# Kernel optimization log

Measured on AMD Instinct MI355X. Metric: run time of the kernel, lower is better.

The kernel has to match this reference:

```python
import jax, jax.numpy as jnp
import numpy as np

TOPK = 6
E = 512
IN = 384
M = 8192
LN_EPS = 1e-5


def _lin(x, w, b):
    # torch nn.Linear: y = x @ W^T + b, W is [out, in]
    return x @ w.T + b


def setup_inputs() -> dict:
    key = jax.random.key(0)
    ks = jax.random.split(key, 16)
    s = lambda k, sh: (jax.random.normal(k, sh, dtype=jnp.float32) * 0.02)
    return {
        "x": jax.random.normal(ks[0], (1, M, IN), dtype=jnp.float32),
        "fc1_w": s(ks[1], (E, IN)), "fc1_b": jnp.zeros((E,), jnp.float32),
        "wh_w": s(ks[2], (E, E)),   "wh_b": jnp.zeros((E,), jnp.float32),
        "wt_w": s(ks[3], (E, E)),   "wt_b": jnp.zeros((E,), jnp.float32),
        "l1_w": s(ks[4], (E, E)),   "l1_b": jnp.zeros((E,), jnp.float32),
        "l2_w": s(ks[5], (E, E)),   "l2_b": jnp.zeros((E,), jnp.float32),
        "a1_w": s(ks[6], (E // 2, E)), "a1_b": jnp.zeros((E // 2,), jnp.float32),
        "a2_w": s(ks[7], (1, E // 2)), "a2_b": jnp.zeros((1,), jnp.float32),
        "ln_g": jnp.ones((E,), jnp.float32), "ln_b": jnp.zeros((E,), jnp.float32),
    }


def reference(x, fc1_w, fc1_b, wh_w, wh_b, wt_w, wt_b,
              l1_w, l1_b, l2_w, l2_b, a1_w, a1_b, a2_w, a2_b, ln_g, ln_b):
    lrelu = jax.nn.leaky_relu  # slope 0.01 == torch default
    h = lrelu(_lin(x, fc1_w, fc1_b))                      # [B,M,E]
    h = (h + h.mean(axis=1, keepdims=True)) * 0.5
    e_h = _lin(h, wh_w, wh_b)                             # [B,M,E]
    e_t = _lin(h, wt_w, wt_b)                             # [B,M,E]
    scale = E ** (-0.5)
    attn_logit = (e_h * scale) @ jnp.swapaxes(e_t, -2, -1)  # [B,M,M]
    topk_weight, topk_index = jax.lax.top_k(attn_logit, TOPK)  # [B,M,K]
    # gather top-k neighbor tail embeddings: [B,M,K,E]
    Nb_h = jax.vmap(lambda et, idx: et[idx])(e_t, topk_index)
    topk_prob = jax.nn.softmax(topk_weight, axis=2)       # [B,M,K]
    eh_r = topk_prob[..., None] * Nb_h + (1.0 - topk_prob)[..., None] * e_h[:, :, None, :]
    gate = jnp.tanh(e_h[:, :, None, :] + eh_r)            # [B,M,K,E]
    # faithful to torch einsum('ijkl,ijkm->ijk'): sums l and m independently
    ka_weight = Nb_h.sum(axis=-1) * gate.sum(axis=-1)     # [B,M,K]
    ka_prob = jax.nn.softmax(ka_weight, axis=2)           # [B,M,K]
    e_Nh = jnp.einsum('bmk,bmke->bme', ka_prob, Nb_h)     # [B,M,E]
    sum_emb = lrelu(_lin(e_h + e_Nh, l1_w, l1_b))
    bi_emb = lrelu(_lin(e_h * e_Nh, l2_w, l2_b))
    emb = sum_emb + bi_emb                                # [B,M,E] (dropout = eval identity)
    hn = emb[0]                                           # squeeze(0) -> [M,E]
    # GeoGlobalAttention readout: gate_nn = Linear->LeakyReLU->Linear, softmax over nodes
    g = _lin(lrelu(_lin(hn, a1_w, a1_b)), a2_w, a2_b)     # [M,1]
    att = jax.nn.softmax(g, axis=0)
    pooled = (att * hn).sum(axis=0, keepdims=True)        # [1,E]
    mu = pooled.mean(axis=-1, keepdims=True)
    var = jnp.mean((pooled - mu) ** 2, axis=-1, keepdims=True)
    out = (pooled - mu) / jnp.sqrt(var + LN_EPS) * ln_g + ln_b
    return out
```

## Files before the change

kernel.cpp:

```cpp
#include <hip/hip_runtime.h>
#include <math.h>
#include <stdint.h>

#define M_NODES 8192
#define E_DIM   512
#define NTOPK   6
#define ATTN_SCALE 0.04419417382415922f
#define NEG_BIG (-1e38f)
#define CAND_CAP 192

typedef __attribute__((ext_vector_type(8))) short short8;
typedef __attribute__((ext_vector_type(4))) float f32x4;

__device__ __forceinline__ float lrelu(float v) { return v > 0.f ? v : 0.01f * v; }

__device__ __forceinline__ unsigned short f2bf(float f) {
  uint32_t u = __float_as_uint(f);
  uint32_t r = (u + 0x7FFFu + ((u >> 16) & 1u)) >> 16;
  return (unsigned short)r;
}
__device__ __forceinline__ float bf2f(unsigned short s) {
  return __uint_as_float(((uint32_t)s) << 16);
}

__device__ __forceinline__ void async_cp16(const void* gptr, void* lds) {
  auto g1 = reinterpret_cast<const __attribute__((address_space(1))) unsigned int*>(
      reinterpret_cast<uintptr_t>(gptr));
  auto l3 = reinterpret_cast<__attribute__((address_space(3))) unsigned int*>(
      reinterpret_cast<uintptr_t>(lds));
  __builtin_amdgcn_global_load_lds(g1, l3, 16, 0, 0);
}



__global__ __launch_bounds__(256) void wcast_kernel(
    const float* __restrict__ x, const float* __restrict__ fc1w,
    const float* __restrict__ whw, const float* __restrict__ wtw,
    const float* __restrict__ l1w, const float* __restrict__ l2w,
    const float* __restrict__ a1w,
    unsigned short* __restrict__ xT, unsigned short* __restrict__ fc1T,
    unsigned short* __restrict__ whT, unsigned short* __restrict__ wtT,
    unsigned short* __restrict__ l1T, unsigned short* __restrict__ l2T,
    unsigned short* __restrict__ a1T)
{
  const int gid = blockIdx.x * 256 + threadIdx.x;
  const float* src; unsigned short* dst; int K8, local;
  if (gid < 417792) {
    K8 = 48;
    if (gid < 393216) { src = x; dst = xT; local = gid; }
    else { src = fc1w; dst = fc1T; local = gid - 393216; }
  } else {
    K8 = 64;
    if (gid < 450560)      { src = whw; dst = whT; local = gid - 417792; }
    else if (gid < 483328) { src = wtw; dst = wtT; local = gid - 450560; }
    else if (gid < 516096) { src = l1w; dst = l1T; local = gid - 483328; }
    else if (gid < 548864) { src = l2w; dst = l2T; local = gid - 516096; }
    else                   { src = a1w; dst = a1T; local = gid - 548864; }
  }
  const int m = local / K8;
  const int k8 = local - m * K8;
  const float* p = src + (size_t)m * (K8 * 8) + k8 * 8;
  float4 v0 = ((const float4*)p)[0];
  float4 v1 = ((const float4*)p)[1];
  const int Kt = K8 >> 2;
  const size_t ti = ((size_t)(m >> 4) * Kt + (k8 >> 2)) * 512 + ((m & 15) + 16 * (k8 & 3)) * 8;
  uint4 pk;
  pk.x = (uint32_t)f2bf(v0.x) | ((uint32_t)f2bf(v0.y) << 16);
  pk.y = (uint32_t)f2bf(v0.z) | ((uint32_t)f2bf(v0.w) << 16);
  pk.z = (uint32_t)f2bf(v1.x) | ((uint32_t)f2bf(v1.y) << 16);
  pk.w = (uint32_t)f2bf(v1.z) | ((uint32_t)f2bf(v1.w) << 16);
  *(uint4*)(dst + ti) = pk;
}

__global__ __launch_bounds__(256, 4) void gemm1_kernel(
    const unsigned short* __restrict__ xT, const unsigned short* __restrict__ fc1T,
    const float* __restrict__ b1, unsigned short* __restrict__ hT,
    float* __restrict__ colsum)
{
  __shared__ unsigned short As[8 * 512];
  __shared__ unsigned short Bs[8 * 512];
  const int tid = threadIdx.x, lane = tid & 63, w = tid >> 6;
  const int wr = w >> 1, wc = w & 1;
  const int m0 = blockIdx.y * 128;
  const int n0 = blockIdx.x * 128;

  f32x4 acc[4][4];
#pragma unroll
  for (int i = 0; i < 4; i++)
#pragma unroll
    for (int j = 0; j < 4; j++) acc[i][j] = (f32x4){0.f, 0.f, 0.f, 0.f};

  for (int kt = 0; kt < 12; kt++) {
    const int s0 = w, s1 = w + 4;
    async_cp16(xT + ((size_t)((m0 >> 4) + s0) * 12 + kt) * 512 + lane * 8, &As[s0 * 512]);
    async_cp16(xT + ((size_t)((m0 >> 4) + s1) * 12 + kt) * 512 + lane * 8, &As[s1 * 512]);
    async_cp16(fc1T + ((size_t)((n0 >> 4) + s0) * 12 + kt) * 512 + lane * 8, &Bs[s0 * 512]);
    async_cp16(fc1T + ((size_t)((n0 >> 4) + s1) * 12 + kt) * 512 + lane * 8, &Bs[s1 * 512]);
    __syncthreads();
    short8 a[4], b[4];
#pragma unroll
    for (int i = 0; i < 4; i++) a[i] = *(const short8*)&As[(wr * 4 + i) * 512 + lane * 8];
#pragma unroll
    for (int j = 0; j < 4; j++) b[j] = *(const short8*)&Bs[(wc * 4 + j) * 512 + lane * 8];
#pragma unroll
    for (int i = 0; i < 4; i++)
#pragma unroll
      for (int j = 0; j < 4; j++)
        acc[i][j] = __builtin_amdgcn_mfma_f32_16x16x32_bf16(a[i], b[j], acc[i][j], 0, 0, 0);
    __syncthreads();
  }

  const int q = lane >> 4, lcol = lane & 15;
  float colp[4] = {};
#pragma unroll
  for (int i = 0; i < 4; i++)
#pragma unroll
    for (int j = 0; j < 4; j++) {
      const int c = n0 + wc * 64 + j * 16 + lcol;
      const float bias = b1[c];
#pragma unroll
      for (int d = 0; d < 4; d++) {
        const int r = m0 + wr * 64 + i * 16 + q * 4 + d;
        const float v = 0.5f * lrelu(acc[i][j][d] + bias);
        hT[((size_t)(r >> 4) * 16 + (c >> 5)) * 512 +
           ((r & 15) + 16 * ((c >> 3) & 3)) * 8 + (c & 7)] = f2bf(v);
        colp[j] += v;
      }
    }
#pragma unroll
  for (int j = 0; j < 4; j++) {
    colp[j] += __shfl_xor(colp[j], 16);
    colp[j] += __shfl_xor(colp[j], 32);
  }
  if (lane < 16) {
#pragma unroll
    for (int j = 0; j < 4; j++)
      atomicAdd(&colsum[n0 + wc * 64 + j * 16 + lcol], colp[j]);
  }
}

__global__ __launch_bounds__(256) void meanproj_kernel(
    const float* __restrict__ colsum, const float* __restrict__ whw,
    const float* __restrict__ wtw, const float* __restrict__ whb,
    const float* __restrict__ wtb, float* __restrict__ biasHT)
{
  const int lane = threadIdx.x & 63;
  const int c1024 = blockIdx.x * 4 + (threadIdx.x >> 6);
  const bool isH = c1024 < 512;
  const int c = isH ? c1024 : c1024 - 512;
  const float* W = (isH ? whw : wtw) + (size_t)c * 512 + lane * 8;
  const float* cs = colsum + lane * 8;
  float s = 0.f;
#pragma unroll
  for (int e = 0; e < 8; e++) s = fmaf(cs[e], W[e], s);
#pragma unroll
  for (int off = 32; off; off >>= 1) s += __shfl_xor(s, off);
  if (lane == 0)
    biasHT[c1024] = (isH ? whb : wtb)[c] + s * (1.f / (float)M_NODES);
}

__global__ __launch_bounds__(256, 4) void dual_gemm(
    const unsigned short* __restrict__ hT, const unsigned short* __restrict__ wstackT,
    const float* __restrict__ biasHT,
    unsigned short* __restrict__ ehT, unsigned short* __restrict__ etT,
    unsigned short* __restrict__ ehRow, unsigned short* __restrict__ etRow)
{
  __shared__ unsigned short As[8 * 512];
  __shared__ unsigned short Bs[8 * 512];
  const int tid = threadIdx.x, lane = tid & 63, w = tid >> 6;
  const int wr = w >> 1, wc = w & 1;
  const int m0 = blockIdx.y * 128;
  const int n0 = blockIdx.x * 128;

  f32x4 acc[4][4];
#pragma unroll
  for (int i = 0; i < 4; i++)
#pragma unroll
    for (int j = 0; j < 4; j++) acc[i][j] = (f32x4){0.f, 0.f, 0.f, 0.f};

  for (int kt = 0; kt < 16; kt++) {
    const int s0 = w, s1 = w + 4;
    async_cp16(hT + ((size_t)((m0 >> 4) + s0) * 16 + kt) * 512 + lane * 8, &As[s0 * 512]);
    async_cp16(hT + ((size_t)((m0 >> 4) + s1) * 16 + kt) * 512 + lane * 8, &As[s1 * 512]);
    async_cp16(wstackT + ((size_t)((n0 >> 4) + s0) * 16 + kt) * 512 + lane * 8, &Bs[s0 * 512]);
    async_cp16(wstackT + ((size_t)((n0 >> 4) + s1) * 16 + kt) * 512 + lane * 8, &Bs[s1 * 512]);
    __syncthreads();
    short8 a[4], b[4];
#pragma unroll
    for (int i = 0; i < 4; i++) a[i] = *(const short8*)&As[(wr * 4 + i) * 512 + lane * 8];
#pragma unroll
    for (int j = 0; j < 4; j++) b[j] = *(const short8*)&Bs[(wc * 4 + j) * 512 + lane * 8];
#pragma unroll
    for (int i = 0; i < 4; i++)
#pragma unroll
      for (int j = 0; j < 4; j++)
        acc[i][j] = __builtin_amdgcn_mfma_f32_16x16x32_bf16(a[i], b[j], acc[i][j], 0, 0, 0);
    __syncthreads();
  }

  const int q = lane >> 4, lcol = lane & 15;
  const bool isH = (n0 < 512);
  const int cb = isH ? n0 : (n0 - 512);
  unsigned short* T = isH ? ehT : etT;
  unsigned short* R = isH ? ehRow : etRow;

#pragma unroll
  for (int i = 0; i < 4; i++)
#pragma unroll
    for (int j = 0; j < 4; j++) {
      const int cl = wc * 64 + j * 16 + lcol;
      const float bias = biasHT[n0 + cl];
      const int c = cb + cl;
#pragma unroll
      for (int d = 0; d < 4; d++) {
        const int r = m0 + wr * 64 + i * 16 + q * 4 + d;
        const unsigned short us = f2bf(acc[i][j][d] + bias);
        T[((size_t)(r >> 4) * 16 + (c >> 5)) * 512 +
          ((r & 15) + 16 * ((c >> 3) & 3)) * 8 + (c & 7)] = us;
        R[(size_t)r * E_DIM + c] = us;
      }
    }
}

template <int MODE>
__global__ __launch_bounds__(256) void mfma_gemm(
    const unsigned short* __restrict__ At1, const unsigned short* __restrict__ At2,
    const unsigned short* __restrict__ Wt1, const unsigned short* __restrict__ Wt2,
    const float* __restrict__ b1, const float* __restrict__ b2,
    float* __restrict__ Cf, unsigned short* __restrict__ T1,
    unsigned short* __restrict__ Cbf, int N, int K)
{
  constexpr bool DUALW = (MODE == 2);
  __shared__ unsigned short As[2][8 * 512];
  __shared__ unsigned short Bs[2][4 * 512];
  const int Kt = K >> 5;
  const int tid = threadIdx.x, lane = tid & 63, w = tid >> 6;
  const int m0 = blockIdx.y * 128, n0 = blockIdx.x * 64;

  f32x4 acc0[2][4], acc1[2][4];
#pragma unroll
  for (int p = 0; p < 2; p++)
#pragma unroll
    for (int j = 0; j < 4; j++) {
      acc0[p][j] = (f32x4){0.f, 0.f, 0.f, 0.f};
      acc1[p][j] = (f32x4){0.f, 0.f, 0.f, 0.f};
    }

  for (int kt = 0; kt < Kt; kt++) {
    const unsigned short* a1p = At1 + ((size_t)((m0 >> 4) + 2 * w) * Kt + kt) * 512 + lane * 8;
    async_cp16(a1p, &As[0][(2 * w) * 512]);
    async_cp16(a1p + (size_t)Kt * 512, &As[0][(2 * w + 1) * 512]);
    if (MODE == 2) {
      const unsigned short* a2p = At2 + ((size_t)((m0 >> 4) + 2 * w) * Kt + kt) * 512 + lane * 8;
      async_cp16(a2p, &As[1][(2 * w) * 512]);
      async_cp16(a2p + (size_t)Kt * 512, &As[1][(2 * w + 1) * 512]);
    }
    const unsigned short* bp1 = Wt1 + ((size_t)((n0 >> 4) + w) * Kt + kt) * 512 + lane * 8;
    async_cp16(bp1, &Bs[0][w * 512]);
    if (DUALW) {
      const unsigned short* bp2 = Wt2 + ((size_t)((n0 >> 4) + w) * Kt + kt) * 512 + lane * 8;
      async_cp16(bp2, &Bs[1][w * 512]);
    }
    __syncthreads();
    short8 a[2], a2[2], bb[4], bb2[4];
#pragma unroll
    for (int p = 0; p < 2; p++) a[p] = *(const short8*)&As[0][(2 * w + p) * 512 + lane * 8];
    if (MODE == 2) {
#pragma unroll
      for (int p = 0; p < 2; p++) a2[p] = *(const short8*)&As[1][(2 * w + p) * 512 + lane * 8];
    }
#pragma unroll
    for (int j = 0; j < 4; j++) bb[j] = *(const short8*)&Bs[0][j * 512 + lane * 8];
    if (DUALW) {
#pragma unroll
      for (int j = 0; j < 4; j++) bb2[j] = *(const short8*)&Bs[1][j * 512 + lane * 8];
    }
#pragma unroll
    for (int p = 0; p < 2; p++)
#pragma unroll
      for (int j = 0; j < 4; j++) {
        acc0[p][j] = __builtin_amdgcn_mfma_f32_16x16x32_bf16(a[p], bb[j], acc0[p][j], 0, 0, 0);
        if (MODE == 2)
          acc1[p][j] = __builtin_amdgcn_mfma_f32_16x16x32_bf16(a2[p], bb2[j], acc1[p][j], 0, 0, 0);
      }
    __syncthreads();
  }

  const int lrow = (lane >> 4) * 4, lcol = lane & 15;

  if (MODE == 3) {
    float part[2][4] = {};
#pragma unroll
    for (int p = 0; p < 2; p++)
#pragma unroll
      for (int j = 0; j < 4; j++) {
        const int c = n0 + j * 16 + lcol;
        const float bias1 = b1[c];
        const float w2 = b2[c];
#pragma unroll
        for (int d = 0; d < 4; d++)
          part[p][d] = fmaf(lrelu(acc0[p][j][d] + bias1), w2, part[p][d]);
      }
#pragma unroll
    for (int p = 0; p < 2; p++)
#pragma unroll
      for (int d = 0; d < 4; d++) {
#pragma unroll
        for (int off = 1; off < 16; off <<= 1)
          part[p][d] += __shfl_xor(part[p][d], off);
      }
    if (lcol == 0) {
#pragma unroll
      for (int p = 0; p < 2; p++)
#pragma unroll
        for (int d = 0; d < 4; d++)
          atomicAdd(&Cf[m0 + w * 32 + p * 16 + lrow + d], part[p][d]);
    }
    return;
  }

  const int NT = N >> 5;
#pragma unroll
  for (int p = 0; p < 2; p++)
#pragma unroll
    for (int j = 0; j < 4; j++) {
      const int c = n0 + j * 16 + lcol;
      const float bias1 = b1[c];
      const float bias2 = b2[c];
#pragma unroll
      for (int d = 0; d < 4; d++) {
        const int r = m0 + w * 32 + p * 16 + lrow + d;
        const float e = lrelu(acc0[p][j][d] + bias1) + lrelu(acc1[p][j][d] + bias2);
        T1[((size_t)(r >> 4) * NT + (c >> 5)) * 512 +
           ((r & 15) + 16 * ((c >> 3) & 3)) * 8 + (c & 7)] = f2bf(e);
        Cbf[(size_t)r * N + c] = f2bf(e);
      }
    }
}

__global__ __launch_bounds__(512, 2) void sgemm_kernel(
    const unsigned short* __restrict__ ehT, const unsigned short* __restrict__ etT,
    unsigned short* __restrict__ sc, float* __restrict__ tmax)
{
  __shared__ unsigned short As[2][32 * 512];
  __shared__ unsigned short Bs[2][32 * 512];
  const int tid = threadIdx.x, lane = tid & 63, w = tid >> 6;
  const int wr = w >> 2, wc = w & 3;
  const int m0 = blockIdx.y * 256;
  const int n0 = blockIdx.x * 256;

  f32x4 acc[8][4];
#pragma unroll
  for (int i = 0; i < 8; i++)
#pragma unroll
    for (int j = 0; j < 4; j++) acc[i][j] = (f32x4){0.f, 0.f, 0.f, 0.f};

  auto stage = [&](int kt) {
    const int bsel = kt & 1;
#pragma unroll
    for (int r = 0; r < 8; r++) {
      const int c = r * 8 + w;
      if (c < 32) {
        async_cp16(ehT + ((size_t)((m0 >> 4) + (c >> 1)) * 16 + (kt * 2 + (c & 1))) * 512 + lane * 8,
                   &As[bsel][c * 512]);
      } else {
        const int c2 = c - 32;
        async_cp16(etT + ((size_t)((n0 >> 4) + (c2 >> 1)) * 16 + (kt * 2 + (c2 & 1))) * 512 + lane * 8,
                   &Bs[bsel][c2 * 512]);
      }
    }
  };

  stage(0);
  stage(1);
  __builtin_amdgcn_sched_barrier(0);
  asm volatile("s_waitcnt vmcnt(8)" ::: "memory");
  __builtin_amdgcn_sched_barrier(0);
  __builtin_amdgcn_s_barrier();

  short8 af[8], bf[8];
  for (int kt = 0; kt < 8; kt++) {
    const int cur = kt & 1;

#pragma unroll
    for (int ii = 0; ii < 4; ii++)
#pragma unroll
      for (int ks = 0; ks < 2; ks++)
        af[ii * 2 + ks] = *(const short8*)&As[cur][((wr * 8 + ii) * 2 + ks) * 512 + lane * 8];
#pragma unroll
    for (int jj = 0; jj < 2; jj++)
#pragma unroll
      for (int ks = 0; ks < 2; ks++)
        bf[jj * 2 + ks] = *(const short8*)&Bs[cur][((wc * 4 + jj) * 2 + ks) * 512 + lane * 8];
    __builtin_amdgcn_s_barrier();
    __builtin_amdgcn_s_setprio(1);
#pragma unroll
    for (int ii = 0; ii < 4; ii++)
#pragma unroll
      for (int jj = 0; jj < 2; jj++)
#pragma unroll
        for (int ks = 0; ks < 2; ks++)
          acc[ii][jj] = __builtin_amdgcn_mfma_f32_16x16x32_bf16(
              af[ii * 2 + ks], bf[jj * 2 + ks], acc[ii][jj], 0, 0, 0);
    __builtin_amdgcn_s_setprio(0);
    __builtin_amdgcn_s_barrier();

#pragma unroll
    for (int jj = 2; jj < 4; jj++)
#pragma unroll
      for (int ks = 0; ks < 2; ks++)
        bf[jj * 2 + ks] = *(const short8*)&Bs[cur][((wc * 4 + jj) * 2 + ks) * 512 + lane * 8];
    __builtin_amdgcn_s_barrier();
    __builtin_amdgcn_s_setprio(1);
#pragma unroll
    for (int ii = 0; ii < 4; ii++)
#pragma unroll
      for (int jj = 2; jj < 4; jj++)
#pragma unroll
        for (int ks = 0; ks < 2; ks++)
          acc[ii][jj] = __builtin_amdgcn_mfma_f32_16x16x32_bf16(
              af[ii * 2 + ks], bf[jj * 2 + ks], acc[ii][jj], 0, 0, 0);
    __builtin_amdgcn_s_setprio(0);
    __builtin_amdgcn_s_barrier();

#pragma unroll
    for (int ii = 0; ii < 4; ii++)
#pragma unroll
      for (int ks = 0; ks < 2; ks++)
        af[ii * 2 + ks] = *(const short8*)&As[cur][((wr * 8 + 4 + ii) * 2 + ks) * 512 + lane * 8];
    __builtin_amdgcn_s_barrier();
    __builtin_amdgcn_s_setprio(1);
#pragma unroll
    for (int ii = 0; ii < 4; ii++)
#pragma unroll
      for (int jj = 2; jj < 4; jj++)
#pragma unroll
        for (int ks = 0; ks < 2; ks++)
          acc[4 + ii][jj] = __builtin_amdgcn_mfma_f32_16x16x32_bf16(
              af[ii * 2 + ks], bf[jj * 2 + ks], acc[4 + ii][jj], 0, 0, 0);
    __builtin_amdgcn_s_setprio(0);
    __builtin_amdgcn_s_barrier();

    if (kt < 6) stage(kt + 2);
    __builtin_amdgcn_s_setprio(1);
#pragma unroll
    for (int ii = 0; ii < 4; ii++)
#pragma unroll
      for (int jj = 0; jj < 2; jj++)
#pragma unroll
        for (int ks = 0; ks < 2; ks++)
          acc[4 + ii][jj] = __builtin_amdgcn_mfma_f32_16x16x32_bf16(
              af[ii * 2 + ks], bf[jj * 2 + ks], acc[4 + ii][jj], 0, 0, 0);
    __builtin_amdgcn_s_setprio(0);

    if (kt < 7) {
      __builtin_amdgcn_sched_barrier(0);
      if (kt < 6) {
        asm volatile("s_waitcnt vmcnt(8)" ::: "memory");
      } else {
        asm volatile("s_waitcnt vmcnt(0)" ::: "memory");
      }
      __builtin_amdgcn_sched_barrier(0);
      __builtin_amdgcn_s_barrier();
    }
  }

  const int q = lane >> 4, lcol = lane & 15;
  const int bn = blockIdx.x * 2 + (wc >> 1);
  const int wcS = wc & 1;

#pragma unroll
  for (int i = 0; i < 8; i++) {
    float rm[4];
#pragma unroll
    for (int d = 0; d < 4; d++) rm[d] = NEG_BIG;
#pragma unroll
    for (int d = 0; d < 4; d++) {
      unsigned short o[4];
#pragma unroll
      for (int j = 0; j < 4; j++) {
        o[j] = f2bf(acc[i][j][d]);
        rm[d] = fmaxf(rm[d], bf2f(o[j]));
      }
      const int row = m0 + wr * 128 + i * 16 + q * 4 + d;
      const size_t off = ((size_t)row * 64 + bn) * 128 + (wcS * 16 + lcol) * 4;
      *(uint2*)(sc + off) = *(uint2*)o;
    }
#pragma unroll
    for (int d = 0; d < 4; d++) {
#pragma unroll
      for (int off2 = 1; off2 < 16; off2 <<= 1)
        rm[d] = fmaxf(rm[d], __shfl_xor(rm[d], off2));
    }
    if (lcol == 0) {
#pragma unroll
      for (int d = 0; d < 4; d++)
        tmax[(size_t)(m0 + wr * 128 + i * 16 + q * 4 + d) * 128 +
             blockIdx.x * 4 + wc] = rm[d];
    }
  }
}

__global__ __launch_bounds__(256) void scan_combine_kernel(
    const unsigned short* __restrict__ sc, const float* __restrict__ tmax,
    const unsigned short* __restrict__ ehRow, const unsigned short* __restrict__ etRow,
    unsigned short* __restrict__ s1T, unsigned short* __restrict__ s2T)
{
  __shared__ float cv[4][CAND_CAP];
  __shared__ int   ci[4][CAND_CAP];
  __shared__ int   cnt[4];
  __shared__ float t6v[4][8];
  __shared__ int   t6i[4][8];
  const int tid = threadIdx.x;
  const int lane = tid & 63;
  const int w = tid >> 6;
  const int row = blockIdx.x * 4 + w;

  if (lane == 0) cnt[w] = 0;
  if (lane < 8) { t6v[w][lane] = 0.f; t6i[w][lane] = 0; }

  const float* tm = tmax + (size_t)row * 128;
  const float v2 = fmaxf(tm[lane], tm[lane + 64]);
  const float bmax = fmaxf(tm[2 * lane], tm[2 * lane + 1]);
  uint32_t u = __float_as_uint(v2);
  u = ((int)u >= 0) ? (u | 0x80000000u) : ~u;
  uint32_t key = (u & ~63u) | (uint32_t)lane;
  float tau = 0.f;
#pragma unroll
  for (int it = 0; it < 6; it++) {
    uint32_t k = key;
#pragma unroll
    for (int off = 32; off; off >>= 1) {
      const uint32_t o = (uint32_t)__shfl_xor((int)k, off);
      k = k > o ? k : o;
    }
    const int wl = (int)(k & 63u);
    if (it == 5) tau = __shfl(v2, wl);
    if (lane == wl) key = 0u;
  }

  unsigned long long mask = __ballot(bmax >= tau);
  const unsigned short* rp = sc + (size_t)row * 8192;
  while (mask) {
    const int bn = __ffsll(mask) - 1;
    mask &= mask - 1;
    const uint32_t uu = *(const uint32_t*)(rp + bn * 128 + lane * 2);
    const float f0 = bf2f((unsigned short)(uu & 0xFFFFu));
    const float f1 = bf2f((unsigned short)(uu >> 16));
#pragma unroll
    for (int e = 0; e < 2; e++) {
      const float f = e ? f1 : f0;
      if (f >= tau) {
        const int idx128 = lane * 2 + e;
        const int g = idx128 >> 2, j = idx128 & 3;
        const int col = bn * 128 + (g >> 4) * 64 + j * 16 + (g & 15);
        const int slot = atomicAdd(&cnt[w], 1);
        if (slot < CAND_CAP) { cv[w][slot] = f; ci[w][slot] = col; }
      }
    }
  }
  __syncthreads();

  int n = cnt[w];
  n = n < CAND_CAP ? n : CAND_CAP;
  for (int c = lane; c < n; c += 64) {
    const float v = cv[w][c];
    const int idx = ci[w][c];
    int rank = 0;
    for (int j = 0; j < n; j++) {
      const float vj = cv[w][j];
      rank += (vj > v) || (vj == v && ci[w][j] < idx);
    }
    if (rank < NTOPK) { t6v[w][rank] = v; t6i[w][rank] = idx; }
  }
  __syncthreads();

  const int m = row;
  float wv[NTOPK]; int id[NTOPK];
#pragma unroll
  for (int k = 0; k < NTOPK; k++) {
    wv[k] = t6v[w][k] * ATTN_SCALE;
    id[k] = t6i[w][k];
  }

  float mx = wv[0];
#pragma unroll
  for (int k = 1; k < NTOPK; k++) mx = fmaxf(mx, wv[k]);
  float p[NTOPK]; float s = 0.f;
#pragma unroll
  for (int k = 0; k < NTOPK; k++) { p[k] = expf(wv[k] - mx); s += p[k]; }
  const float inv = 1.f / s;
#pragma unroll
  for (int k = 0; k < NTOPK; k++) p[k] *= inv;

  short8 eh8 = *(const short8*)(ehRow + (size_t)m * E_DIM + lane * 8);
  float ehv[8];
#pragma unroll
  for (int e = 0; e < 8; e++) ehv[e] = bf2f((unsigned short)eh8[e]);

  float nv[NTOPK][8];
#pragma unroll
  for (int k = 0; k < NTOPK; k++) {
    short8 nb = *(const short8*)(etRow + (size_t)id[k] * E_DIM + lane * 8);
#pragma unroll
    for (int e = 0; e < 8; e++) nv[k][e] = bf2f((unsigned short)nb[e]);
  }

  float ka[NTOPK];
#pragma unroll
  for (int k = 0; k < NTOPK; k++) {
    float snb = 0.f, sg = 0.f;
    const float aa = 2.f - p[k], bb = p[k];
#pragma unroll
    for (int e = 0; e < 8; e++) {
      snb += nv[k][e];
      sg += tanhf(fmaf(aa, ehv[e], bb * nv[k][e]));
    }
#pragma unroll
    for (int off = 32; off; off >>= 1) {
      snb += __shfl_xor(snb, off);
      sg += __shfl_xor(sg, off);
    }
    ka[k] = snb * sg;
  }
  float km = ka[0];
#pragma unroll
  for (int k = 1; k < NTOPK; k++) km = fmaxf(km, ka[k]);
  float kp[NTOPK]; float ks = 0.f;
#pragma unroll
  for (int k = 0; k < NTOPK; k++) { kp[k] = expf(ka[k] - km); ks += kp[k]; }
  const float kinv = 1.f / ks;

  const size_t tbase = ((size_t)(m >> 4) * 16 + (lane >> 2)) * 512 +
                       ((m & 15) + 16 * (lane & 3)) * 8;
  unsigned short o1[8], o2[8];
#pragma unroll
  for (int e = 0; e < 8; e++) {
    float o = 0.f;
#pragma unroll
    for (int k = 0; k < NTOPK; k++) o = fmaf(kp[k], nv[k][e], o);
    o *= kinv;
    o1[e] = f2bf(ehv[e] + o);
    o2[e] = f2bf(ehv[e] * o);
  }
  *(short8*)(s1T + tbase) = *(short8*)o1;
  *(short8*)(s2T + tbase) = *(short8*)o2;
}

__global__ __launch_bounds__(256) void pooled_kernel(
    const unsigned short* __restrict__ emb, const float* __restrict__ g,
    float* __restrict__ pooled, float* __restrict__ wsum)
{
  const int t = threadIdx.x;
  const int r0 = blockIdx.x * 128;
  float a0 = 0.f, a1 = 0.f, lsum = 0.f;
  for (int r = 0; r < 128; r++) {
    const int m = r0 + r;
    const float wv = expf(g[m]);
    lsum += wv;
    a0 = fmaf(wv, bf2f(emb[(size_t)m * E_DIM + t]), a0);
    a1 = fmaf(wv, bf2f(emb[(size_t)m * E_DIM + 256 + t]), a1);
  }
  atomicAdd(&pooled[t], a0);
  atomicAdd(&pooled[t + 256], a1);
  if (t == 0) atomicAdd(wsum, lsum);
}

__global__ __launch_bounds__(512) void ln_kernel(
    const float* __restrict__ pooled, const float* __restrict__ wsum,
    const float* __restrict__ lng, const float* __restrict__ lnb,
    float* __restrict__ out)
{
  __shared__ float red[8];
  __shared__ float red2[8];
  const int t = threadIdx.x;
  const float v = pooled[t] / wsum[0];
  float s = v;
#pragma unroll
  for (int off = 32; off; off >>= 1) s += __shfl_xor(s, off);
  if ((t & 63) == 0) red[t >> 6] = s;
  __syncthreads();
  float tot = 0.f;
  for (int i = 0; i < 8; i++) tot += red[i];
  const float mu = tot / (float)E_DIM;
  const float d = v - mu;
  float q = d * d;
#pragma unroll
  for (int off = 32; off; off >>= 1) q += __shfl_xor(q, off);
  if ((t & 63) == 0) red2[t >> 6] = q;
  __syncthreads();
  float vt = 0.f;
  for (int i = 0; i < 8; i++) vt += red2[i];
  const float var = vt / (float)E_DIM;
  out[t] = d * rsqrtf(var + 1e-5f) * lng[t] + lnb[t];
}

extern "C" void kernel_launch(void* const* d_in, const int* in_sizes, int n_in,
                              void* d_out, int out_size, void* d_ws, size_t ws_size,
                              hipStream_t stream)
{
  const float* x     = (const float*)d_in[0];
  const float* fc1_w = (const float*)d_in[1];
  const float* fc1_b = (const float*)d_in[2];
  const float* wh_w  = (const float*)d_in[3];
  const float* wh_b  = (const float*)d_in[4];
  const float* wt_w  = (const float*)d_in[5];
  const float* wt_b  = (const float*)d_in[6];
  const float* l1_w  = (const float*)d_in[7];
  const float* l1_b  = (const float*)d_in[8];
  const float* l2_w  = (const float*)d_in[9];
  const float* l2_b  = (const float*)d_in[10];
  const float* a1_w  = (const float*)d_in[11];
  const float* a1_b  = (const float*)d_in[12];
  const float* a2_w  = (const float*)d_in[13];
  const float* a2_b  = (const float*)d_in[14];
  const float* ln_g  = (const float*)d_in[15];
  const float* ln_b  = (const float*)d_in[16];
  (void)a2_b;

  char* ws = (char*)d_ws;
  const size_t MiB = 1 << 20;
  unsigned short* fc1T = (unsigned short*)(ws + 0);
  unsigned short* whT  = (unsigned short*)(ws + 393216);
  unsigned short* wtT  = (unsigned short*)(ws + 917504);
  unsigned short* l1T  = (unsigned short*)(ws + 1441792);
  unsigned short* l2T  = (unsigned short*)(ws + 1966080);
  unsigned short* a1T  = (unsigned short*)(ws + 2490368);
  unsigned short* xT     = (unsigned short*)(ws + 3 * MiB);
  unsigned short* hT     = (unsigned short*)(ws + 25 * MiB);
  unsigned short* ehT    = (unsigned short*)(ws + 33 * MiB);
  unsigned short* etT    = (unsigned short*)(ws + 41 * MiB);
  unsigned short* ehRow  = (unsigned short*)(ws + 49 * MiB);
  unsigned short* etRow  = (unsigned short*)(ws + 57 * MiB);
  float*          tmaxb  = (float*)(ws + 65 * MiB);
  unsigned short* s1T    = (unsigned short*)(ws + 3 * MiB);
  unsigned short* s2T    = (unsigned short*)(ws + 11 * MiB);
  unsigned short* embT   = (unsigned short*)(ws + 19 * MiB);
  unsigned short* embRow = (unsigned short*)(ws + 27 * MiB);
  unsigned short* scores = (unsigned short*)(ws + 96 * MiB);
  char*           smal   = ws + 69 * MiB;
  float* colsum = (float*)(smal);
  float* biasHT = (float*)(smal + 2048);
  float* g      = (float*)(smal + 8192);
  float* stats  = (float*)(smal + 40960);
  float* pooled = (float*)(smal + 45056);

  hipMemsetAsync(smal, 0, 47104, stream);

  wcast_kernel<<<2208, 256, 0, stream>>>(x, fc1_w, wh_w, wt_w, l1_w, l2_w, a1_w,
                                         xT, fc1T, whT, wtT, l1T, l2T, a1T);
  gemm1_kernel<<<dim3(4, 64), 256, 0, stream>>>(xT, fc1T, fc1_b, hT, colsum);
  meanproj_kernel<<<256, 256, 0, stream>>>(colsum, wh_w, wt_w, wh_b, wt_b, biasHT);
  dual_gemm<<<dim3(8, 64), 256, 0, stream>>>(hT, whT, biasHT, ehT, etT, ehRow, etRow);
  sgemm_kernel<<<dim3(32, 32), 512, 0, stream>>>(ehT, etT, scores, tmaxb);
  scan_combine_kernel<<<M_NODES / 4, 256, 0, stream>>>(
      scores, tmaxb, ehRow, etRow, s1T, s2T);
  mfma_gemm<2><<<dim3(8, 64), 256, 0, stream>>>(
      s1T, s2T, l1T, l2T, l1_b, l2_b, nullptr, embT, embRow, 512, 512);
  mfma_gemm<3><<<dim3(4, 64), 256, 0, stream>>>(
      embT, nullptr, a1T, nullptr, a1_b, a2_w, g, nullptr, nullptr, 256, 512);
  pooled_kernel<<<64, 256, 0, stream>>>(embRow, g, pooled, stats);
  ln_kernel<<<1, 512, 0, stream>>>(pooled, stats, ln_g, ln_b, (float*)d_out);
}
```

Baseline: 299.2 us.

## Swizzle GEMM block order and interleave prefetch copies across MFMA phases

The score GEMM now remaps the flat block index so that consecutively scheduled blocks share operand row and column tiles, aiming to improve L2 reuse. It also splits the single prefetch of the k+2 stage into chunks issued across the three MFMA phases. Each chunk is issued only after every wave has finished reading that region of the shared buffer, so global-to-LDS copies overlap with compute instead of bunching at one point. The risks are the tight buffer-reuse ordering, which relies on existing barriers, and extra address arithmetic.

```diff
diff --git a/kernel.cpp b/kernel.cpp
--- a/kernel.cpp
+++ b/kernel.cpp
@@ -346,8 +346,11 @@
   __shared__ unsigned short Bs[2][32 * 512];
   const int tid = threadIdx.x, lane = tid & 63, w = tid >> 6;
   const int wr = w >> 2, wc = w & 3;
-  const int m0 = blockIdx.y * 256;
-  const int n0 = blockIdx.x * 256;
+  const int f  = blockIdx.y * 32 + blockIdx.x;
+  const int fp = (f & 7) * 128 + (f >> 3);
+  const int bx = fp & 31, by = fp >> 5;
+  const int m0 = by * 256;
+  const int n0 = bx * 256;
 
   f32x4 acc[8][4];
 #pragma unroll
@@ -355,24 +358,25 @@
 #pragma unroll
     for (int j = 0; j < 4; j++) acc[i][j] = (f32x4){0.f, 0.f, 0.f, 0.f};
 
-  auto stage = [&](int kt) {
+  auto stage_chunk = [&](int kt, int cc) {
     const int bsel = kt & 1;
-#pragma unroll
-    for (int r = 0; r < 8; r++) {
-      const int c = r * 8 + w;
-      if (c < 32) {
-        async_cp16(ehT + ((size_t)((m0 >> 4) + (c >> 1)) * 16 + (kt * 2 + (c & 1))) * 512 + lane * 8,
-                   &As[bsel][c * 512]);
-      } else {
-        const int c2 = c - 32;
-        async_cp16(etT + ((size_t)((n0 >> 4) + (c2 >> 1)) * 16 + (kt * 2 + (c2 & 1))) * 512 + lane * 8,
-                   &Bs[bsel][c2 * 512]);
-      }
+    if (cc < 32) {
+      async_cp16(ehT + ((size_t)((m0 >> 4) + (cc >> 1)) * 16 + (kt * 2 + (cc & 1))) * 512 + lane * 8,
+                 &As[bsel][cc * 512]);
+    } else {
+      const int c2 = cc - 32;
+      async_cp16(etT + ((size_t)((n0 >> 4) + (c2 >> 1)) * 16 + (kt * 2 + (c2 & 1))) * 512 + lane * 8,
+                 &Bs[bsel][c2 * 512]);
     }
   };
-
-  stage(0);
-  stage(1);
+  auto stage_all = [&](int kt) {
+#pragma unroll
+    for (int r = 0; r < 8; r++) stage_chunk(kt, r * 8 + w);
+  };
+  const int wp = w + (w & 4);
+
+  stage_all(0);
+  stage_all(1);
   __builtin_amdgcn_sched_barrier(0);
   asm volatile("s_waitcnt vmcnt(8)" ::: "memory");
   __builtin_amdgcn_sched_barrier(0);
@@ -410,6 +414,11 @@
 #pragma unroll
       for (int ks = 0; ks < 2; ks++)
         bf[jj * 2 + ks] = *(const short8*)&Bs[cur][((wc * 4 + jj) * 2 + ks) * 512 + lane * 8];
+    if (kt < 6) {
+      stage_chunk(kt + 2, w);
+      stage_chunk(kt + 2, 16 + w);
+      stage_chunk(kt + 2, 32 + wp);
+    }
     __builtin_amdgcn_s_barrier();
     __builtin_amdgcn_s_setprio(1);
 #pragma unroll
@@ -428,6 +437,11 @@
 #pragma unroll
       for (int ks = 0; ks < 2; ks++)
         af[ii * 2 + ks] = *(const short8*)&As[cur][((wr * 8 + 4 + ii) * 2 + ks) * 512 + lane * 8];
+    if (kt < 6) {
+      stage_chunk(kt + 2, 48 + wp);
+      stage_chunk(kt + 2, 36 + wp);
+      stage_chunk(kt + 2, 52 + wp);
+    }
     __builtin_amdgcn_s_barrier();
     __builtin_amdgcn_s_setprio(1);
 #pragma unroll
@@ -441,7 +455,10 @@
     __builtin_amdgcn_s_setprio(0);
     __builtin_amdgcn_s_barrier();
 
-    if (kt < 6) stage(kt + 2);
+    if (kt < 6) {
+      stage_chunk(kt + 2, 8 + w);
+      stage_chunk(kt + 2, 24 + w);
+    }
     __builtin_amdgcn_s_setprio(1);
 #pragma unroll
     for (int ii = 0; ii < 4; ii++)
@@ -466,7 +483,7 @@
   }
 
   const int q = lane >> 4, lcol = lane & 15;
-  const int bn = blockIdx.x * 2 + (wc >> 1);
+  const int bn = bx * 2 + (wc >> 1);
   const int wcS = wc & 1;
 
 #pragma unroll
@@ -496,7 +513,7 @@
 #pragma unroll
       for (int d = 0; d < 4; d++)
         tmax[(size_t)(m0 + wr * 128 + i * 16 + q * 4 + d) * 128 +
-             blockIdx.x * 4 + wc] = rm[d];
+             bx * 4 + wc] = rm[d];
     }
   }
 }
```

Result: slower. 308.3 us (+3.0%).
